# Kernel tuning notes

Hardware: AMD Instinct MI355X
Metric: run time of the kernel (lower is better)

Reference implementation:

```python
import jax, jax.numpy as jnp
import numpy as np

WINDOW_SIZE = 11
SIGMA = 1.5
C1 = 0.0001
C2 = 0.0009


def _gaussian_kernel(window_size, channels):
    # 1D gaussian, sigma=1.5 (standard SSIM window), normalized
    ax = np.arange(window_size, dtype=np.float32) - (window_size - 1) / 2.0
    g = np.exp(-(ax ** 2) / (2.0 * SIGMA ** 2))
    g = g / g.sum()
    k2d = np.outer(g, g).astype(np.float32)  # [w, w], sums to 1
    # depthwise kernel, OIHW with groups=channels -> [C, 1, w, w]
    return jnp.asarray(np.tile(k2d[None, None], (channels, 1, 1, 1)))


def _dwconv(x, kernel):
    p = WINDOW_SIZE // 2
    return jax.lax.conv_general_dilated(
        x, kernel,
        window_strides=(1, 1),
        padding=[(p, p), (p, p)],
        dimension_numbers=('NCHW', 'OIHW', 'NCHW'),
        feature_group_count=x.shape[1],
    )


def setup_inputs() -> dict:
    key = jax.random.key(0)
    k1, k2 = jax.random.split(key)
    B, C, H, W = 16, 3, 512, 512
    x = jax.random.uniform(k1, (B, C, H, W), dtype=jnp.float32)
    y = jax.random.uniform(k2, (B, C, H, W), dtype=jnp.float32)
    return {"x": x, "y": y}


def reference(x, y):
    kernel = _gaussian_kernel(WINDOW_SIZE, x.shape[1])
    mean_sr = _dwconv(x, kernel)
    mean_hr = _dwconv(y, kernel)
    mean_sr_sq = mean_sr * mean_sr
    mean_hr_sq = mean_hr * mean_hr
    var_sr = _dwconv(x * x, kernel) - mean_sr_sq
    var_hr = _dwconv(y * y, kernel) - mean_hr_sq
    covar = _dwconv(x * y, kernel) - mean_sr * mean_hr
    ssim_pix = ((2.0 * mean_sr * mean_hr + C1) * (2.0 * covar + C2)
                / ((mean_sr_sq + mean_hr_sq + C1) * (var_sr + var_hr + C2)))
    ssim_mean = jnp.mean(ssim_pix)
    loss = -jnp.log10(ssim_mean)
    return (loss, ssim_mean)
```

## Files before the change

kernel.cpp:

```cpp
#include <hip/hip_runtime.h>
#include <hip/hip_fp16.h>
#include <math.h>

#define IMG   512
#define TWD   64
#define BROWS 32
#define WIN   42
#define HS2   34
#define NBLK  6144
#define NPIX  12582912.0

constexpr float G[11] = {
    0.00102838f, 0.00759876f, 0.03600077f, 0.10936069f, 0.21300554f,
    0.26601173f,
    0.21300554f, 0.10936069f, 0.03600077f, 0.00759876f, 0.00102838f};

template<bool MASKED>
__device__ __forceinline__ void conv_store(
    __half2 (&hb2)[4][WIN][HS2],
    const float4 (&fx)[6], const float4 (&fy)[6],
    int grow, int gc0, int bufrow, int hg)
{
    float gm[6];
#pragma unroll
    for (int i = 0; i < 6; ++i) {
        if (MASKED) {
            const float rm = ((unsigned)grow < IMG) ? 1.f : 0.f;
            gm[i] = ((unsigned)(gc0 + 4 * i) < IMG) ? rm : 0.f;
        } else {
            gm[i] = 1.f;
        }
    }
    float ax[8] = {}, ay[8] = {}, ass[8] = {}, axy[8] = {};
#pragma unroll
    for (int i = 0; i < 6; ++i) {
        const float vx4[4] = {fx[i].x, fx[i].y, fx[i].z, fx[i].w};
        const float vy4[4] = {fy[i].x, fy[i].y, fy[i].z, fy[i].w};
#pragma unroll
        for (int c = 0; c < 4; ++c) {
            const int j = 4 * i + c;
            if (j < 3 || j > 20) continue;
            const float a  = MASKED ? vx4[c] * gm[i] : vx4[c];
            const float b  = MASKED ? vy4[c] * gm[i] : vy4[c];
            const float ss = fmaf(a, a, b * b);
            const float xy = a * b;
#pragma unroll
            for (int e = 0; e < 8; ++e) {
                const int k = j - 3 - e;
                if (k >= 0 && k <= 10) {
                    ax[e]  = fmaf(G[k], a,  ax[e]);
                    ay[e]  = fmaf(G[k], b,  ay[e]);
                    ass[e] = fmaf(G[k], ss, ass[e]);
                    axy[e] = fmaf(G[k], xy, axy[e]);
                }
            }
        }
    }
    const int p0 = 4 * hg;
#pragma unroll
    for (int p = 0; p < 4; ++p) {
        hb2[0][bufrow][p0 + p] = __floats2half2_rn(ax[2*p],  ax[2*p+1]);
        hb2[1][bufrow][p0 + p] = __floats2half2_rn(ay[2*p],  ay[2*p+1]);
        hb2[2][bufrow][p0 + p] = __floats2half2_rn(ass[2*p], ass[2*p+1]);
        hb2[3][bufrow][p0 + p] = __floats2half2_rn(axy[2*p], axy[2*p+1]);
    }
}

template<bool MASKED>
__device__ __forceinline__ void htask(
    __half2 (&hb2)[4][WIN][HS2],
    const float* __restrict__ xb, const float* __restrict__ yb,
    int rbase0, int c0, int t)
{
    const int brow = t >> 3, g = t & 7;
    const int grow = rbase0 - 5 + brow;
    const int gc0  = c0 - 8 + 8 * g;
    float4 fx[6], fy[6];
    if (MASKED) {
        const float* __restrict__ px = xb + min(max(grow, 0), IMG - 1) * IMG;
        const float* __restrict__ py = yb + min(max(grow, 0), IMG - 1) * IMG;
#pragma unroll
        for (int i = 0; i < 6; ++i) {
            int gcl = min(max(gc0 + 4 * i, 0), IMG - 4);
            fx[i] = *(const float4*)(px + gcl);
            fy[i] = *(const float4*)(py + gcl);
        }
    } else {
        const float* __restrict__ px = xb + grow * IMG + gc0;
        const float* __restrict__ py = yb + grow * IMG + gc0;
#pragma unroll
        for (int i = 0; i < 6; ++i) {
            fx[i] = *(const float4*)(px + 4 * i);
            fy[i] = *(const float4*)(py + 4 * i);
        }
    }
    conv_store<MASKED>(hb2, fx, fy, grow, gc0, brow, g);
}

__device__ __forceinline__ float vpass16(
    const __half2 (&hb2)[4][WIN][HS2], const __half2 (&Gh)[11],
    int rb, int cg)
{
    __half2 vr[4][4];
    const __half2 z2 = __floats2half2_rn(0.f, 0.f);
#pragma unroll
    for (int q = 0; q < 4; ++q)
#pragma unroll
        for (int j = 0; j < 4; ++j) vr[q][j] = z2;
#pragma unroll
    for (int q = 0; q < 4; ++q)
#pragma unroll
        for (int k = 0; k < 14; ++k) {
            __half2 v = hb2[q][rb + k][cg];
#pragma unroll
            for (int j = 0; j < 4; ++j)
                if (k - j >= 0 && k - j <= 10)
                    vr[q][j] = __hfma2(Gh[k - j], v, vr[q][j]);
        }
    float s = 0.f;
#pragma unroll
    for (int j = 0; j < 4; ++j) {
        float2 mxv  = __half22float2(vr[0][j]);
        float2 myv  = __half22float2(vr[1][j]);
        float2 mssv = __half22float2(vr[2][j]);
        float2 mxyv = __half22float2(vr[3][j]);
        const float mxa[2]  = {mxv.x, mxv.y};
        const float mya[2]  = {myv.x, myv.y};
        const float mssa[2] = {mssv.x, mssv.y};
        const float mxya[2] = {mxyv.x, mxyv.y};
#pragma unroll
        for (int e = 0; e < 2; ++e) {
            float mx = mxa[e], my = mya[e];
            float mss = mssa[e], mxy = mxya[e];
            float mx2 = mx * mx, my2 = my * my, mxmy = mx * my;
            float num = (2.f * mxmy + 0.0001f) * (2.f * (mxy - mxmy) + 0.0009f);
            float den = (mx2 + my2 + 0.0001f) * ((mss - mx2 - my2) + 0.0009f);
            s += num * __builtin_amdgcn_rcpf(den);
        }
    }
    return s;
}

__global__ __launch_bounds__(256) void ssim_tile_kernel(
    const float* __restrict__ x, const float* __restrict__ y,
    float* __restrict__ partial)
{
    __shared__ __half2 hb2[4][WIN][HS2];
    __shared__ float wsum[4];

    const int tid = threadIdx.x;
    const int bid = blockIdx.x;
    const int nb  = (bid & 7) * (NBLK / 8) + (bid >> 3);
    const int z   = nb >> 7;
    const int rem = nb & 127;
    const int by  = rem >> 3, bx = rem & 7;
    const int c0 = bx * TWD;
    const int rbase0 = by * BROWS;
    const size_t ioff = (size_t)z * IMG * IMG;
    const float* __restrict__ xb = x + ioff;
    const float* __restrict__ yb = y + ioff;

    const bool interior = (bx >= 1) & (bx <= 6) & (by >= 1) & (by <= 14);

    __half2 Gh[11];
#pragma unroll
    for (int k = 0; k < 11; ++k) Gh[k] = __floats2half2_rn(G[k], G[k]);

    if (interior) {
        htask<false>(hb2, xb, yb, rbase0, c0, tid);
        if (tid < 80) htask<false>(hb2, xb, yb, rbase0, c0, tid + 256);
    } else {
        htask<true>(hb2, xb, yb, rbase0, c0, tid);
        if (tid < 80) htask<true>(hb2, xb, yb, rbase0, c0, tid + 256);
    }
    __syncthreads();

    const int cg = tid & 31;
    const int rb = (tid >> 5) * 4;
    float lsum = vpass16(hb2, Gh, rb, cg);

#pragma unroll
    for (int off = 32; off > 0; off >>= 1)
        lsum += __shfl_down(lsum, off, 64);
    if ((tid & 63) == 0) wsum[tid >> 6] = lsum;
    __syncthreads();
    if (tid == 0)
        partial[bid] = wsum[0] + wsum[1] + wsum[2] + wsum[3];
}

__global__ __launch_bounds__(1024) void ssim_reduce_kernel(
    const float* __restrict__ partial, float* __restrict__ out)
{
    __shared__ double ws[16];
    const int tid = threadIdx.x;
    double s = 0.0;
#pragma unroll
    for (int i = 0; i < NBLK / 1024; ++i) s += (double)partial[tid + i * 1024];
#pragma unroll
    for (int off = 32; off > 0; off >>= 1)
        s += __shfl_down(s, off, 64);
    if ((tid & 63) == 0) ws[tid >> 6] = s;
    __syncthreads();
    if (tid == 0) {
        double t = 0.0;
#pragma unroll
        for (int w = 0; w < 16; ++w) t += ws[w];
        double mean = t / NPIX;
        out[0] = (float)(-log10(mean));
        out[1] = (float)mean;
    }
}

extern "C" void kernel_launch(void* const* d_in, const int* in_sizes, int n_in,
                              void* d_out, int out_size, void* d_ws, size_t ws_size,
                              hipStream_t stream)
{
    const float* x = (const float*)d_in[0];
    const float* y = (const float*)d_in[1];
    float* out     = (float*)d_out;
    float* partial = (float*)d_ws;

    ssim_tile_kernel<<<NBLK, 256, 0, stream>>>(x, y, partial);
    ssim_reduce_kernel<<<1, 1024, 0, stream>>>(partial, out);
}
```

Measured before the change: 55.21 us.

## Process four vertical strips per block, reusing halo rows and prefetching next strip

Each block now walks four 32-row strips of a 64-column tile, 128 rows in all. Between strips it copies the 10 overlapping horizontally-filtered halo rows within shared memory rather than recomputing them. While the current strip's vertical pass runs, it prefetches the next strip's new input rows into registers. This cuts redundant halo loads and horizontal convolution, but leaves a quarter as many blocks and adds extra barriers per strip, which may reduce parallelism and latency hiding.

```diff
diff --git a/kernel.cpp b/kernel.cpp
--- a/kernel.cpp
+++ b/kernel.cpp
@@ -2,18 +2,44 @@
 #include <hip/hip_fp16.h>
 #include <math.h>
 
-#define IMG   512
-#define TWD   64
-#define BROWS 32
-#define WIN   42
-#define HS2   34
-#define NBLK  6144
-#define NPIX  12582912.0
+#define IMG    512
+#define TWD    64
+#define NSTRIP 4
+#define BROWS  128
+#define WIN    42
+#define HS2    34
+#define NBLK   1536
+#define NPIX   12582912.0
 
 constexpr float G[11] = {
     0.00102838f, 0.00759876f, 0.03600077f, 0.10936069f, 0.21300554f,
     0.26601173f,
     0.21300554f, 0.10936069f, 0.03600077f, 0.00759876f, 0.00102838f};
+
+template<bool MASKED>
+__device__ __forceinline__ void issue_loads(
+    const float* __restrict__ xb, const float* __restrict__ yb,
+    int grow, int gc0, float4 (&fx)[6], float4 (&fy)[6])
+{
+    if (MASKED) {
+        const float* __restrict__ px = xb + min(max(grow, 0), IMG - 1) * IMG;
+        const float* __restrict__ py = yb + min(max(grow, 0), IMG - 1) * IMG;
+#pragma unroll
+        for (int i = 0; i < 6; ++i) {
+            int gcl = min(max(gc0 + 4 * i, 0), IMG - 4);
+            fx[i] = *(const float4*)(px + gcl);
+            fy[i] = *(const float4*)(py + gcl);
+        }
+    } else {
+        const float* __restrict__ px = xb + grow * IMG + gc0;
+        const float* __restrict__ py = yb + grow * IMG + gc0;
+#pragma unroll
+        for (int i = 0; i < 6; ++i) {
+            fx[i] = *(const float4*)(px + 4 * i);
+            fy[i] = *(const float4*)(py + 4 * i);
+        }
+    }
+}
 
 template<bool MASKED>
 __device__ __forceinline__ void conv_store(
@@ -27,9 +53,7 @@
         if (MASKED) {
             const float rm = ((unsigned)grow < IMG) ? 1.f : 0.f;
             gm[i] = ((unsigned)(gc0 + 4 * i) < IMG) ? rm : 0.f;
-        } else {
-            gm[i] = 1.f;
-        }
+        } else gm[i] = 1.f;
     }
     float ax[8] = {}, ay[8] = {}, ass[8] = {}, axy[8] = {};
 #pragma unroll
@@ -67,7 +91,7 @@
 }
 
 template<bool MASKED>
-__device__ __forceinline__ void htask(
+__device__ __forceinline__ void fill_task(
     __half2 (&hb2)[4][WIN][HS2],
     const float* __restrict__ xb, const float* __restrict__ yb,
     int rbase0, int c0, int t)
@@ -76,24 +100,7 @@
     const int grow = rbase0 - 5 + brow;
     const int gc0  = c0 - 8 + 8 * g;
     float4 fx[6], fy[6];
-    if (MASKED) {
-        const float* __restrict__ px = xb + min(max(grow, 0), IMG - 1) * IMG;
-        const float* __restrict__ py = yb + min(max(grow, 0), IMG - 1) * IMG;
-#pragma unroll
-        for (int i = 0; i < 6; ++i) {
-            int gcl = min(max(gc0 + 4 * i, 0), IMG - 4);
-            fx[i] = *(const float4*)(px + gcl);
-            fy[i] = *(const float4*)(py + gcl);
-        }
-    } else {
-        const float* __restrict__ px = xb + grow * IMG + gc0;
-        const float* __restrict__ py = yb + grow * IMG + gc0;
-#pragma unroll
-        for (int i = 0; i < 6; ++i) {
-            fx[i] = *(const float4*)(px + 4 * i);
-            fy[i] = *(const float4*)(py + 4 * i);
-        }
-    }
+    issue_loads<MASKED>(xb, yb, grow, gc0, fx, fy);
     conv_store<MASKED>(hb2, fx, fy, grow, gc0, brow, g);
 }
 
@@ -151,8 +158,8 @@
     const int tid = threadIdx.x;
     const int bid = blockIdx.x;
     const int nb  = (bid & 7) * (NBLK / 8) + (bid >> 3);
-    const int z   = nb >> 7;
-    const int rem = nb & 127;
+    const int z   = nb >> 5;
+    const int rem = nb & 31;
     const int by  = rem >> 3, bx = rem & 7;
     const int c0 = bx * TWD;
     const int rbase0 = by * BROWS;
@@ -160,24 +167,60 @@
     const float* __restrict__ xb = x + ioff;
     const float* __restrict__ yb = y + ioff;
 
-    const bool interior = (bx >= 1) & (bx <= 6) & (by >= 1) & (by <= 14);
+    const bool xmask = (bx == 0) | (bx == 7);
 
     __half2 Gh[11];
 #pragma unroll
     for (int k = 0; k < 11; ++k) Gh[k] = __floats2half2_rn(G[k], G[k]);
 
-    if (interior) {
-        htask<false>(hb2, xb, yb, rbase0, c0, tid);
-        if (tid < 80) htask<false>(hb2, xb, yb, rbase0, c0, tid + 256);
+    const int hrow = tid >> 3;
+    const int hg   = tid & 7;
+    const int gc0  = c0 - 8 + 8 * hg;
+    const int cg   = tid & 31;
+    const int rb   = (tid >> 5) * 4;
+    float lsum = 0.f;
+
+    float4 pfx[6], pfy[6];
+
+    if (xmask | (by == 0)) {
+        fill_task<true>(hb2, xb, yb, rbase0, c0, tid);
+        if (tid < 80) fill_task<true>(hb2, xb, yb, rbase0, c0, tid + 256);
     } else {
-        htask<true>(hb2, xb, yb, rbase0, c0, tid);
-        if (tid < 80) htask<true>(hb2, xb, yb, rbase0, c0, tid + 256);
-    }
-    __syncthreads();
-
-    const int cg = tid & 31;
-    const int rb = (tid >> 5) * 4;
-    float lsum = vpass16(hb2, Gh, rb, cg);
+        fill_task<false>(hb2, xb, yb, rbase0, c0, tid);
+        if (tid < 80) fill_task<false>(hb2, xb, yb, rbase0, c0, tid + 256);
+    }
+    if (xmask) issue_loads<true >(xb, yb, rbase0 + 37 + hrow, gc0, pfx, pfy);
+    else       issue_loads<false>(xb, yb, rbase0 + 37 + hrow, gc0, pfx, pfy);
+    __syncthreads();
+    lsum += vpass16(hb2, Gh, rb, cg);
+    __syncthreads();
+
+#pragma unroll
+    for (int s = 1; s < NSTRIP; ++s) {
+        const int sbase = rbase0 + 32 * s;
+#pragma unroll
+        for (int k = 0; k < 3; ++k) {
+            int idx = tid + k * 256;
+            if (idx < 640) {
+                int q = idx / 160, rr = (idx - q * 160) >> 4, p = idx & 15;
+                *(float2*)&hb2[q][rr][2 * p] =
+                    *(const float2*)&hb2[q][32 + rr][2 * p];
+            }
+        }
+        __syncthreads();
+        const bool smask = xmask | ((by == 3) & (s == 3));
+        if (smask) conv_store<true >(hb2, pfx, pfy, sbase + 5 + hrow, gc0, 10 + hrow, hg);
+        else       conv_store<false>(hb2, pfx, pfy, sbase + 5 + hrow, gc0, 10 + hrow, hg);
+        if (s < NSTRIP - 1) {
+            const int ngrow = rbase0 + 32 * (s + 1) + 5 + hrow;
+            const bool nmask = xmask | ((by == 3) & (s + 1 == 3));
+            if (nmask) issue_loads<true >(xb, yb, ngrow, gc0, pfx, pfy);
+            else       issue_loads<false>(xb, yb, ngrow, gc0, pfx, pfy);
+        }
+        __syncthreads();
+        lsum += vpass16(hb2, Gh, rb, cg);
+        __syncthreads();
+    }
 
 #pragma unroll
     for (int off = 32; off > 0; off >>= 1)
@@ -194,8 +237,7 @@
     __shared__ double ws[16];
     const int tid = threadIdx.x;
     double s = 0.0;
-#pragma unroll
-    for (int i = 0; i < NBLK / 1024; ++i) s += (double)partial[tid + i * 1024];
+    for (int i = tid; i < NBLK; i += 1024) s += (double)partial[i];
 #pragma unroll
     for (int off = 32; off > 0; off >>= 1)
         s += __shfl_down(s, off, 64);
```

Measured after the change: 96.47 us. 1.75x slower.
